# Performance work log

Hardware: AMD Instinct MI355X
Metric: run time of the kernel (lower is better)

The kernel has to match this reference:

```python
import jax, jax.numpy as jnp
import numpy as np

WIN = (7, 7)
NUM_HEADS = 12
LORA_SCALING = 16.0 / 16.0  # lora_alpha / lora_rank


def _relative_position_index(win):
    wh, ww = win
    coords = np.stack(np.meshgrid(np.arange(wh), np.arange(ww), indexing='ij'))  # (2, wh, ww)
    cf = coords.reshape(2, -1)
    rel = cf[:, :, None] - cf[:, None, :]  # (2, N, N)
    rel = rel.transpose(1, 2, 0)
    rel[:, :, 0] += wh - 1
    rel[:, :, 1] += ww - 1
    rel[:, :, 0] *= 2 * ww - 1
    return jnp.asarray(rel.sum(-1), dtype=jnp.int32)  # (N, N)


def setup_inputs() -> dict:
    key = jax.random.key(0)
    ks = jax.random.split(key, 12)
    B_, N, C, r = 2048, 49, 384, 16
    nW = 64
    s = 0.02
    return {
        'x': jax.random.normal(ks[0], (B_, N, C), jnp.float32),
        'mask': jnp.zeros((nW, N, N), jnp.float32),
        'qkv_w': jax.random.normal(ks[1], (C, 3 * C), jnp.float32) * s,
        'qkv_b': jax.random.normal(ks[2], (3 * C,), jnp.float32) * s,
        'qa_w': jax.random.normal(ks[3], (C, r), jnp.float32) * s,
        'qb_w': jax.random.normal(ks[4], (r, C), jnp.float32) * s,
        'va_w': jax.random.normal(ks[5], (C, r), jnp.float32) * s,
        'vb_w': jax.random.normal(ks[6], (r, C), jnp.float32) * s,
        'rpb_table': jax.random.normal(ks[7], ((2 * WIN[0] - 1) * (2 * WIN[1] - 1), NUM_HEADS), jnp.float32) * s,
        'proj_w': jax.random.normal(ks[8], (C, C), jnp.float32) * s,
        'proj_b': jax.random.normal(ks[9], (C,), jnp.float32) * s,
    }


def reference(x, mask, qkv_w, qkv_b, qa_w, qb_w, va_w, vb_w, rpb_table, proj_w, proj_b):
    B_, N, C = x.shape
    H = NUM_HEADS
    hd = C // H
    scale = hd ** -0.5

    qkv = (x @ qkv_w + qkv_b).reshape(B_, N, 3, H, hd)
    qkv = jnp.transpose(qkv, (2, 0, 3, 1, 4))  # (3, B_, H, N, hd)
    q, k, v = qkv[0], qkv[1], qkv[2]

    q_lora = LORA_SCALING * ((x @ qa_w) @ qb_w)  # (B_, N, C)
    q = q + jnp.transpose(q_lora.reshape(B_, N, H, hd), (0, 2, 1, 3))
    v_lora = LORA_SCALING * ((x @ va_w) @ vb_w)
    v = v + jnp.transpose(v_lora.reshape(B_, N, H, hd), (0, 2, 1, 3))

    attn = jnp.einsum('bhnd,bhmd->bhnm', q * scale, k)  # (B_, H, N, N)

    rel_idx = _relative_position_index(WIN)  # (N, N) static int
    rpb = rpb_table[rel_idx]  # (N, N, H)
    attn = attn + jnp.transpose(rpb, (2, 0, 1))[None]

    nW = mask.shape[0]
    attn = attn.reshape(B_ // nW, nW, H, N, N) + mask[None, :, None]
    attn = attn.reshape(B_, H, N, N)
    attn = jax.nn.softmax(attn, axis=-1)

    out = jnp.einsum('bhnm,bhmd->bhnd', attn, v)
    out = jnp.transpose(out, (0, 2, 1, 3)).reshape(B_, N, C)
    return out @ proj_w + proj_b
```

## Files before the change

kernel.cpp:

```cpp
#include <hip/hip_runtime.h>
#include <hip/hip_bf16.h>

typedef __hip_bfloat16 bf16;
typedef float f32x4 __attribute__((ext_vector_type(4)));
typedef short bf16x8 __attribute__((ext_vector_type(8)));

static __device__ __forceinline__ void gload_lds16(const void* g, void* l) {
    __builtin_amdgcn_global_load_lds(
        (const __attribute__((address_space(1))) void*)g,
        (__attribute__((address_space(3))) void*)l, 16, 0, 0);
}

static __device__ __forceinline__ short bf16bits(float v) {
    bf16 tb = __float2bfloat16(v);
    return *reinterpret_cast<short*>(&tb);
}

__global__ __launch_bounds__(256) void cvt_x_kernel(const float4* __restrict__ x,
                                                    bf16* __restrict__ xb, int n4) {
    int i = blockIdx.x * 256 + threadIdx.x;
    const int stride = gridDim.x * 256;
    for (; i < n4; i += stride) {
        float4 v = x[i];
        alignas(8) bf16 tmp[4];
        tmp[0] = __float2bfloat16(v.x);
        tmp[1] = __float2bfloat16(v.y);
        tmp[2] = __float2bfloat16(v.z);
        tmp[3] = __float2bfloat16(v.w);
        *reinterpret_cast<uint2*>(xb + 4l * i) = *reinterpret_cast<uint2*>(tmp);
    }
}

__global__ __launch_bounds__(256) void build_wefft_kernel(
    const float* __restrict__ qkv_w, const float* __restrict__ qa,
    const float* __restrict__ qb, const float* __restrict__ va,
    const float* __restrict__ vb, bf16* __restrict__ wt) {
    int idx = blockIdx.x * 256 + threadIdx.x;
    int ncol = idx / 384;
    int k = idx - ncol * 384;
    float v = qkv_w[k * 1152 + ncol];
    if (ncol < 384) {
        float s = 0.f;
#pragma unroll
        for (int j = 0; j < 16; ++j) s += qa[k * 16 + j] * qb[j * 384 + ncol];
        v += s;
    } else if (ncol >= 768) {
        int nc = ncol - 768;
        float s = 0.f;
#pragma unroll
        for (int j = 0; j < 16; ++j) s += va[k * 16 + j] * vb[j * 384 + nc];
        v += s;
    }
    wt[(long)ncol * 384 + k] = __float2bfloat16(v);
}

__global__ __launch_bounds__(256) void build_projt_kernel(const float* __restrict__ pw,
                                                          bf16* __restrict__ pt) {
    int idx = blockIdx.x * 256 + threadIdx.x;
    int ncol = idx / 384;
    int k = idx - ncol * 384;
    pt[(long)ncol * 384 + k] = __float2bfloat16(pw[k * 384 + ncol]);
}

__global__ __launch_bounds__(256) void build_cbias_kernel(const float* __restrict__ rpb_table,
                                                          const float* __restrict__ mask,
                                                          float* __restrict__ cbias) {
    int idx = blockIdx.x * 256 + threadIdx.x;
    int hw = idx / 2401;
    int ij = idx - hw * 2401;
    int h = hw >> 6, w = hw & 63;
    int i = ij / 49, j = ij - i * 49;
    int yi = i / 7, xi = i - yi * 7;
    int yj = j / 7, xj = j - yj * 7;
    int rel = (yi - yj + 6) * 13 + (xi - xj + 6);
    cbias[idx] = rpb_table[rel * 12 + h] + mask[w * 2401 + ij];
}

template <bool OUT_BF16>
__global__ __launch_bounds__(256) void gemm_kernel(const bf16* __restrict__ A,
                                                   const bf16* __restrict__ BT,
                                                   const float* __restrict__ bias,
                                                   void* __restrict__ Cout,
                                                   int N, int K, int nxb, int nwg) {
    __shared__ short Al[128 * 64];
    __shared__ short Bl[128 * 64];
    const int t = threadIdx.x;
    const int lane = t & 63;
    const int wave = t >> 6;
    const int wr = wave >> 1;
    const int wc = wave & 1;
    const int g = lane >> 4, c = lane & 15;

    const int q8 = nwg >> 3;
    const int wgid = (blockIdx.x & 7) * q8 + (blockIdx.x >> 3);
    const int by = wgid / nxb;
    const int bx = wgid - by * nxb;
    const long rowBase = (long)by * 128;
    const long colBase = (long)bx * 128;

    f32x4 acc[4][4];
#pragma unroll
    for (int m = 0; m < 4; ++m)
#pragma unroll
        for (int n = 0; n < 4; ++n) acc[m][n] = (f32x4){0.f, 0.f, 0.f, 0.f};

    for (int k0 = 0; k0 < K; k0 += 64) {
        __syncthreads();
#pragma unroll
        for (int it = 0; it < 4; ++it) {
            int chunk = it * 256 + t;
            int row = chunk >> 3;
            int blk = lane & 7;
            gload_lds16(A + (size_t)(rowBase + row) * K + k0 + ((blk ^ (row & 7)) * 8),
                        &Al[(it * 256 + wave * 64) * 8]);
            gload_lds16(BT + (size_t)(colBase + row) * K + k0 + ((blk ^ (row & 7)) * 8),
                        &Bl[(it * 256 + wave * 64) * 8]);
        }
        asm volatile("s_waitcnt vmcnt(0)" ::: "memory");
        __syncthreads();

#pragma unroll
        for (int ks = 0; ks < 2; ++ks) {
            bf16x8 af[4], bfr[4];
#pragma unroll
            for (int m = 0; m < 4; ++m) {
                int row = wr * 64 + m * 16 + c;
                af[m] = *(const bf16x8*)&Al[row * 64 + (((ks * 4 + g) ^ (c & 7)) * 8)];
            }
#pragma unroll
            for (int n = 0; n < 4; ++n) {
                int row = wc * 64 + n * 16 + c;
                bfr[n] = *(const bf16x8*)&Bl[row * 64 + (((ks * 4 + g) ^ (c & 7)) * 8)];
            }
#pragma unroll
            for (int m = 0; m < 4; ++m)
#pragma unroll
                for (int n = 0; n < 4; ++n)
                    acc[m][n] = __builtin_amdgcn_mfma_f32_16x16x32_bf16(af[m], bfr[n],
                                                                        acc[m][n], 0, 0, 0);
        }
    }

    const int crow0 = wr * 64 + g * 4;
    const long ccol0 = colBase + wc * 64 + c;
#pragma unroll
    for (int m = 0; m < 4; ++m) {
#pragma unroll
        for (int n = 0; n < 4; ++n) {
            const long col = ccol0 + n * 16;
            const float bv = bias[col];
#pragma unroll
            for (int r = 0; r < 4; ++r) {
                const long row = rowBase + crow0 + m * 16 + r;
                float v = acc[m][n][r] + bv;
                if (OUT_BF16)
                    ((bf16*)Cout)[row * N + col] = __float2bfloat16(v);
                else
                    ((float*)Cout)[row * N + col] = v;
            }
        }
    }
}

__global__ __launch_bounds__(256) void attn_kernel(const bf16* __restrict__ qkv,
                                                   const float* __restrict__ cbias,
                                                   bf16* __restrict__ out) {
    __shared__ short lds[4 * 7168];
    const int t = threadIdx.x, lane = t & 63, wave = t >> 6;
    short* W = lds + wave * 7168;
    const int bh = blockIdx.x * 4 + wave;
    const int b = bh / 12, h = bh - b * 12;
    const int g = lane >> 4, c = lane & 15;
    const int w = b & 63;

    const size_t base = (size_t)b * 49 * 1152 + h * 32;
    uint4 qr[3], kr[3], vr[3];
#pragma unroll
    for (int it = 0; it < 3; ++it) {
        int c4 = it * 64 + lane;
        int n = c4 >> 2, o = (c4 & 3) * 8;
        const bf16* src = qkv + base + (size_t)n * 1152 + o;
        qr[it] = *(const uint4*)(src);
        kr[it] = *(const uint4*)(src + 384);
        vr[it] = *(const uint4*)(src + 768);
    }
    uint4 qt4, kt4, vt4;
    {
        const bf16* src = qkv + base + (size_t)48 * 1152 + (lane & 3) * 8;
        qt4 = *(const uint4*)(src);
        kt4 = *(const uint4*)(src + 384);
        vt4 = *(const uint4*)(src + 768);
    }

#pragma unroll
    for (int z = 0; z < 4; ++z)
        *(uint4*)&W[5120 + (z * 64 + lane) * 8] = (uint4){0u, 0u, 0u, 0u};

#pragma unroll
    for (int it = 0; it < 3; ++it) {
        int c4 = it * 64 + lane;
        int n = c4 >> 2, o = (c4 & 3) * 8;
        *(uint4*)&W[n * 40 + o] = qr[it];
        *(uint4*)&W[2560 + n * 40 + o] = kr[it];
        alignas(16) short tmp[8];
        *(uint4*)tmp = vr[it];
#pragma unroll
        for (int j = 0; j < 8; ++j) {
            int d = o + j;
            W[5120 + ((d * 64 + n) ^ ((d & 7) << 3))] = tmp[j];
        }
    }
    if (lane < 4) {
        int o = (lane & 3) * 8;
        *(uint4*)&W[48 * 40 + o] = qt4;
        *(uint4*)&W[2560 + 48 * 40 + o] = kt4;
        alignas(16) short tmp[8];
        *(uint4*)tmp = vt4;
#pragma unroll
        for (int j = 0; j < 8; ++j) {
            int d = o + j;
            W[5120 + ((d * 64 + 48) ^ ((d & 7) << 3))] = tmp[j];
        }
    }
    __syncthreads();

    bf16x8 aq[4], bk[4];
#pragma unroll
    for (int mt = 0; mt < 4; ++mt) aq[mt] = *(const bf16x8*)&W[(mt * 16 + c) * 40 + g * 8];
#pragma unroll
    for (int nt = 0; nt < 4; ++nt) bk[nt] = *(const bf16x8*)&W[2560 + (nt * 16 + c) * 40 + g * 8];
    f32x4 S[4][4];
#pragma unroll
    for (int mt = 0; mt < 4; ++mt)
#pragma unroll
        for (int nt = 0; nt < 4; ++nt)
            S[mt][nt] = __builtin_amdgcn_mfma_f32_16x16x32_bf16(aq[mt], bk[nt],
                                                                (f32x4){0.f, 0.f, 0.f, 0.f}, 0, 0, 0);

    const float scale = 0.17677669529663687f;
    const float* cb = cbias + (size_t)((h << 6) | w) * 2401;
    float inv[16];
#pragma unroll
    for (int mt = 0; mt < 4; ++mt) {
#pragma unroll
        for (int nt = 0; nt < 4; ++nt) {
            int j = nt * 16 + c;
#pragma unroll
            for (int r = 0; r < 4; ++r) {
                int i = mt * 16 + g * 4 + r;
                float v = S[mt][nt][r] * scale;
                if (j < 49 && i < 49) v += cb[i * 49 + j];
                S[mt][nt][r] = (j < 49) ? v : -INFINITY;
            }
        }
#pragma unroll
        for (int r = 0; r < 4; ++r) {
            float m = fmaxf(fmaxf(S[mt][0][r], S[mt][1][r]), fmaxf(S[mt][2][r], S[mt][3][r]));
            m = fmaxf(m, __shfl_xor(m, 1));
            m = fmaxf(m, __shfl_xor(m, 2));
            m = fmaxf(m, __shfl_xor(m, 4));
            m = fmaxf(m, __shfl_xor(m, 8));
            float s = 0.f;
#pragma unroll
            for (int nt = 0; nt < 4; ++nt) {
                float e = __expf(S[mt][nt][r] - m);
                S[mt][nt][r] = e;
                s += e;
            }
            s += __shfl_xor(s, 1);
            s += __shfl_xor(s, 2);
            s += __shfl_xor(s, 4);
            s += __shfl_xor(s, 8);
            inv[mt * 4 + r] = 1.f / s;
        }
    }

    __syncthreads();
#pragma unroll
    for (int mt = 0; mt < 4; ++mt)
#pragma unroll
        for (int r = 0; r < 4; ++r) {
            const int i = mt * 16 + g * 4 + r;
            const int ix = (i & 7) << 3;
#pragma unroll
            for (int nt = 0; nt < 4; ++nt) {
                unsigned my = (unsigned)(unsigned short)bf16bits(S[mt][nt][r]);
                unsigned oth = (unsigned)__builtin_amdgcn_mov_dpp((int)my, 0xB1, 0xF, 0xF, true);
                unsigned pair = (c & 1) ? (oth | (my << 16)) : (my | (oth << 16));
                const bool doit = (c & 1) ? (nt >= 2) : (nt < 2);
                if (doit) {
                    int j0 = nt * 16 + (c & ~1);
                    *(unsigned*)&W[i * 64 + (j0 ^ ix)] = pair;
                }
            }
        }
    __syncthreads();

    f32x4 O[4][2];
#pragma unroll
    for (int mt = 0; mt < 4; ++mt)
#pragma unroll
        for (int dt = 0; dt < 2; ++dt) O[mt][dt] = (f32x4){0.f, 0.f, 0.f, 0.f};
#pragma unroll
    for (int ks = 0; ks < 2; ++ks) {
        bf16x8 pa[4], vb2[2];
#pragma unroll
        for (int mt = 0; mt < 4; ++mt) {
            int i = mt * 16 + c;
            pa[mt] = *(const bf16x8*)&W[(i * 64 + ks * 32 + g * 8) ^ ((i & 7) << 3)];
        }
#pragma unroll
        for (int dt = 0; dt < 2; ++dt) {
            int d = dt * 16 + c;
            vb2[dt] = *(const bf16x8*)&W[5120 + ((d * 64 + ks * 32 + g * 8) ^ ((d & 7) << 3))];
        }
#pragma unroll
        for (int mt = 0; mt < 4; ++mt)
#pragma unroll
            for (int dt = 0; dt < 2; ++dt)
                O[mt][dt] = __builtin_amdgcn_mfma_f32_16x16x32_bf16(pa[mt], vb2[dt],
                                                                    O[mt][dt], 0, 0, 0);
    }

#pragma unroll
    for (int mt = 0; mt < 4; ++mt)
#pragma unroll
        for (int r = 0; r < 4; ++r) {
            int i = mt * 16 + g * 4 + r;
            if (i < 49) {
#pragma unroll
                for (int dt = 0; dt < 2; ++dt) {
                    int d = dt * 16 + c;
                    out[((size_t)(b * 49 + i)) * 384 + h * 32 + d] =
                        __float2bfloat16(O[mt][dt][r] * inv[mt * 4 + r]);
                }
            }
        }
}

extern "C" void kernel_launch(void* const* d_in, const int* in_sizes, int n_in,
                              void* d_out, int out_size, void* d_ws, size_t ws_size,
                              hipStream_t stream) {
    (void)in_sizes; (void)n_in; (void)out_size; (void)ws_size;
    const float* x      = (const float*)d_in[0];
    const float* mask   = (const float*)d_in[1];
    const float* qkv_w  = (const float*)d_in[2];
    const float* qkv_b  = (const float*)d_in[3];
    const float* qa_w   = (const float*)d_in[4];
    const float* qb_w   = (const float*)d_in[5];
    const float* va_w   = (const float*)d_in[6];
    const float* vb_w   = (const float*)d_in[7];
    const float* rpb    = (const float*)d_in[8];
    const float* proj_w = (const float*)d_in[9];
    const float* proj_b = (const float*)d_in[10];

    char* ws = (char*)d_ws;
    bf16* xb     = (bf16*)(ws);
    bf16* attno  = (bf16*)(ws);
    bf16* wefft  = (bf16*)(ws + 77070336);
    bf16* projt  = (bf16*)(ws + 77955072);
    float* cbias = (float*)(ws + 78249984);
    bf16* qkv    = (bf16*)(ws + 85625856);

    cvt_x_kernel<<<2048, 256, 0, stream>>>((const float4*)x, xb, 9633792);
    build_wefft_kernel<<<1728, 256, 0, stream>>>(qkv_w, qa_w, qb_w, va_w, vb_w, wefft);
    build_projt_kernel<<<576, 256, 0, stream>>>(proj_w, projt);
    build_cbias_kernel<<<7203, 256, 0, stream>>>(rpb, mask, cbias);
    gemm_kernel<true><<<7056, 256, 0, stream>>>(xb, wefft, qkv_b, qkv, 1152, 384, 9, 7056);
    attn_kernel<<<6144, 256, 0, stream>>>(qkv, cbias, attno);
    gemm_kernel<false><<<2352, 256, 0, stream>>>(attno, projt, proj_b, d_out, 384, 384, 3, 2352);
}
```

Measured before the change: 399.9 us.

## Load Q/K fragments straight to registers in attention and drop barriers

The attention kernel now loads Q and K MFMA operands directly from global memory into registers instead of staging them through LDS. Padded rows are clamped to row 48, so those lanes read valid data. Scores are computed per row-tile and written as P immediately, and V is transposed into LDS afterwards, which removes both block barriers and shrinks LDS per block. Separately, the QKV projection GEMM is split into two half-size launches, which adds a launch with no clear benefit.

New measurement: 392.8 us. Within noise of the previous version (-1.8%).

```diff
diff --git a/kernel.cpp b/kernel.cpp
--- a/kernel.cpp
+++ b/kernel.cpp
@@ -165,97 +165,61 @@
 __global__ __launch_bounds__(256) void attn_kernel(const bf16* __restrict__ qkv,
                                                    const float* __restrict__ cbias,
                                                    bf16* __restrict__ out) {
-    __shared__ short lds[4 * 7168];
+    __shared__ short lds[4 * 6144];
     const int t = threadIdx.x, lane = t & 63, wave = t >> 6;
-    short* W = lds + wave * 7168;
+    short* W = lds + wave * 6144;
     const int bh = blockIdx.x * 4 + wave;
     const int b = bh / 12, h = bh - b * 12;
     const int g = lane >> 4, c = lane & 15;
     const int w = b & 63;
-
     const size_t base = (size_t)b * 49 * 1152 + h * 32;
-    uint4 qr[3], kr[3], vr[3];
+    const float scale = 0.17677669529663687f;
+
+    uint4 vr[3], vt4;
 #pragma unroll
     for (int it = 0; it < 3; ++it) {
         int c4 = it * 64 + lane;
         int n = c4 >> 2, o = (c4 & 3) * 8;
-        const bf16* src = qkv + base + (size_t)n * 1152 + o;
-        qr[it] = *(const uint4*)(src);
-        kr[it] = *(const uint4*)(src + 384);
-        vr[it] = *(const uint4*)(src + 768);
-    }
-    uint4 qt4, kt4, vt4;
-    {
-        const bf16* src = qkv + base + (size_t)48 * 1152 + (lane & 3) * 8;
-        qt4 = *(const uint4*)(src);
-        kt4 = *(const uint4*)(src + 384);
-        vt4 = *(const uint4*)(src + 768);
+        vr[it] = *(const uint4*)(qkv + base + (size_t)n * 1152 + 768 + o);
+    }
+    vt4 = *(const uint4*)(qkv + base + (size_t)48 * 1152 + 768 + (lane & 3) * 8);
+
+    bf16x8 aq[4], bk[4];
+#pragma unroll
+    for (int mt = 0; mt < 4; ++mt) {
+        int row = mt * 16 + c;
+        row = row > 48 ? 48 : row;
+        aq[mt] = *(const bf16x8*)(qkv + base + (size_t)row * 1152 + g * 8);
+        bk[mt] = *(const bf16x8*)(qkv + base + (size_t)row * 1152 + 384 + g * 8);
     }
 
 #pragma unroll
     for (int z = 0; z < 4; ++z)
-        *(uint4*)&W[5120 + (z * 64 + lane) * 8] = (uint4){0u, 0u, 0u, 0u};
-
-#pragma unroll
-    for (int it = 0; it < 3; ++it) {
-        int c4 = it * 64 + lane;
-        int n = c4 >> 2, o = (c4 & 3) * 8;
-        *(uint4*)&W[n * 40 + o] = qr[it];
-        *(uint4*)&W[2560 + n * 40 + o] = kr[it];
-        alignas(16) short tmp[8];
-        *(uint4*)tmp = vr[it];
-#pragma unroll
-        for (int j = 0; j < 8; ++j) {
-            int d = o + j;
-            W[5120 + ((d * 64 + n) ^ ((d & 7) << 3))] = tmp[j];
-        }
-    }
-    if (lane < 4) {
-        int o = (lane & 3) * 8;
-        *(uint4*)&W[48 * 40 + o] = qt4;
-        *(uint4*)&W[2560 + 48 * 40 + o] = kt4;
-        alignas(16) short tmp[8];
-        *(uint4*)tmp = vt4;
-#pragma unroll
-        for (int j = 0; j < 8; ++j) {
-            int d = o + j;
-            W[5120 + ((d * 64 + 48) ^ ((d & 7) << 3))] = tmp[j];
-        }
-    }
-    __syncthreads();
-
-    bf16x8 aq[4], bk[4];
-#pragma unroll
-    for (int mt = 0; mt < 4; ++mt) aq[mt] = *(const bf16x8*)&W[(mt * 16 + c) * 40 + g * 8];
-#pragma unroll
-    for (int nt = 0; nt < 4; ++nt) bk[nt] = *(const bf16x8*)&W[2560 + (nt * 16 + c) * 40 + g * 8];
-    f32x4 S[4][4];
-#pragma unroll
-    for (int mt = 0; mt < 4; ++mt)
-#pragma unroll
-        for (int nt = 0; nt < 4; ++nt)
-            S[mt][nt] = __builtin_amdgcn_mfma_f32_16x16x32_bf16(aq[mt], bk[nt],
-                                                                (f32x4){0.f, 0.f, 0.f, 0.f}, 0, 0, 0);
-
-    const float scale = 0.17677669529663687f;
+        *(uint4*)&W[4096 + (z * 64 + lane) * 8] = (uint4){0u, 0u, 0u, 0u};
+
     const float* cb = cbias + (size_t)((h << 6) | w) * 2401;
     float inv[16];
 #pragma unroll
     for (int mt = 0; mt < 4; ++mt) {
+        f32x4 Sv[4];
+#pragma unroll
+        for (int nt = 0; nt < 4; ++nt)
+            Sv[nt] = __builtin_amdgcn_mfma_f32_16x16x32_bf16(aq[mt], bk[nt],
+                                                             (f32x4){0.f, 0.f, 0.f, 0.f}, 0, 0, 0);
 #pragma unroll
         for (int nt = 0; nt < 4; ++nt) {
             int j = nt * 16 + c;
 #pragma unroll
             for (int r = 0; r < 4; ++r) {
                 int i = mt * 16 + g * 4 + r;
-                float v = S[mt][nt][r] * scale;
+                float v = Sv[nt][r] * scale;
                 if (j < 49 && i < 49) v += cb[i * 49 + j];
-                S[mt][nt][r] = (j < 49) ? v : -INFINITY;
+                Sv[nt][r] = (j < 49) ? v : -INFINITY;
             }
         }
 #pragma unroll
         for (int r = 0; r < 4; ++r) {
-            float m = fmaxf(fmaxf(S[mt][0][r], S[mt][1][r]), fmaxf(S[mt][2][r], S[mt][3][r]));
+            float m = fmaxf(fmaxf(Sv[0][r], Sv[1][r]), fmaxf(Sv[2][r], Sv[3][r]));
             m = fmaxf(m, __shfl_xor(m, 1));
             m = fmaxf(m, __shfl_xor(m, 2));
             m = fmaxf(m, __shfl_xor(m, 4));
@@ -263,8 +227,8 @@
             float s = 0.f;
 #pragma unroll
             for (int nt = 0; nt < 4; ++nt) {
-                float e = __expf(S[mt][nt][r] - m);
-                S[mt][nt][r] = e;
+                float e = __expf(Sv[nt][r] - m);
+                Sv[nt][r] = e;
                 s += e;
             }
             s += __shfl_xor(s, 1);
@@ -273,18 +237,13 @@
             s += __shfl_xor(s, 8);
             inv[mt * 4 + r] = 1.f / s;
         }
-    }
-
-    __syncthreads();
-#pragma unroll
-    for (int mt = 0; mt < 4; ++mt)
 #pragma unroll
         for (int r = 0; r < 4; ++r) {
             const int i = mt * 16 + g * 4 + r;
             const int ix = (i & 7) << 3;
 #pragma unroll
             for (int nt = 0; nt < 4; ++nt) {
-                unsigned my = (unsigned)(unsigned short)bf16bits(S[mt][nt][r]);
+                unsigned my = (unsigned)(unsigned short)bf16bits(Sv[nt][r]);
                 unsigned oth = (unsigned)__builtin_amdgcn_mov_dpp((int)my, 0xB1, 0xF, 0xF, true);
                 unsigned pair = (c & 1) ? (oth | (my << 16)) : (my | (oth << 16));
                 const bool doit = (c & 1) ? (nt >= 2) : (nt < 2);
@@ -294,7 +253,30 @@
                 }
             }
         }
-    __syncthreads();
+    }
+
+#pragma unroll
+    for (int it = 0; it < 3; ++it) {
+        int c4 = it * 64 + lane;
+        int n = c4 >> 2, o = (c4 & 3) * 8;
+        alignas(16) short tmp[8];
+        *(uint4*)tmp = vr[it];
+#pragma unroll
+        for (int j = 0; j < 8; ++j) {
+            int d = o + j;
+            W[4096 + ((d * 64 + n) ^ ((d & 7) << 3))] = tmp[j];
+        }
+    }
+    if (lane < 4) {
+        int o = (lane & 3) * 8;
+        alignas(16) short tmp[8];
+        *(uint4*)tmp = vt4;
+#pragma unroll
+        for (int j = 0; j < 8; ++j) {
+            int d = o + j;
+            W[4096 + ((d * 64 + 48) ^ ((d & 7) << 3))] = tmp[j];
+        }
+    }
 
     f32x4 O[4][2];
 #pragma unroll
@@ -312,7 +294,7 @@
 #pragma unroll
         for (int dt = 0; dt < 2; ++dt) {
             int d = dt * 16 + c;
-            vb2[dt] = *(const bf16x8*)&W[5120 + ((d * 64 + ks * 32 + g * 8) ^ ((d & 7) << 3))];
+            vb2[dt] = *(const bf16x8*)&W[4096 + ((d * 64 + ks * 32 + g * 8) ^ ((d & 7) << 3))];
         }
 #pragma unroll
         for (int mt = 0; mt < 4; ++mt)
@@ -366,7 +348,9 @@
     build_wefft_kernel<<<1728, 256, 0, stream>>>(qkv_w, qa_w, qb_w, va_w, vb_w, wefft);
     build_projt_kernel<<<576, 256, 0, stream>>>(proj_w, projt);
     build_cbias_kernel<<<7203, 256, 0, stream>>>(rpb, mask, cbias);
-    gemm_kernel<true><<<7056, 256, 0, stream>>>(xb, wefft, qkv_b, qkv, 1152, 384, 9, 7056);
+    gemm_kernel<true><<<3528, 256, 0, stream>>>(xb, wefft, qkv_b, qkv, 1152, 384, 9, 3528);
+    gemm_kernel<true><<<3528, 256, 0, stream>>>(xb + (size_t)50176 * 384, wefft, qkv_b,
+                                                qkv + (size_t)50176 * 1152, 1152, 384, 9, 3528);
     attn_kernel<<<6144, 256, 0, stream>>>(qkv, cbias, attno);
     gemm_kernel<false><<<2352, 256, 0, stream>>>(attno, projt, proj_b, d_out, 384, 384, 3, 2352);
 }
```
